# Performance work log

Hardware: AMD Instinct MI355X
Metric: run time of the kernel (lower is better)

## Reference

```python
import jax, jax.numpy as jnp
import numpy as np

B, S, E, H, FFN, NQ, DEPTH = 2, 2048, 1024, 16, 4096, 4, 2
DK = E // H
LN_EPS = 1e-5


def _layernorm(t, g, b):
    m = t.mean(-1, keepdims=True)
    v = ((t - m) ** 2).mean(-1, keepdims=True)
    return (t - m) / jnp.sqrt(v + LN_EPS) * g + b


def setup_inputs() -> dict:
    key = jax.random.key(0)
    ks = jax.random.split(key, 12)
    n = lambda i, shape, sc=1.0: (jax.random.normal(ks[i], shape, jnp.float32) * sc)
    return {
        "x": n(0, (B, S, E)),
        "wq": n(1, (E, E), 0.02),
        "wk": n(2, (E, E), 0.02),
        "wv": n(3, (E, E), 0.02),
        "wo": n(4, (E, E), 0.02),
        "w1": n(5, (E, FFN), 0.02),
        "b1": jnp.zeros((FFN,), jnp.float32),
        "w2": n(6, (FFN, E), 0.02),
        "b2": jnp.zeros((E,), jnp.float32),
        "qp_attn": n(7, (NQ, DEPTH)),
        "qp_ffn": n(8, (NQ, DEPTH)),
        "ln1_g": jnp.ones((E,), jnp.float32),
        "ln1_b": jnp.zeros((E,), jnp.float32),
        "ln2_g": jnp.ones((E,), jnp.float32),
        "ln2_b": jnp.zeros((E,), jnp.float32),
    }


def reference(x, wq, wk, wv, wo, w1, b1, w2, b2, qp_attn, qp_ffn,
              ln1_g, ln1_b, ln2_g, ln2_b):
    b, s, _ = x.shape
    # --- quantum attention ---
    q = (x @ wq).reshape(b, s, H, DK)
    k = (x @ wk).reshape(b, s, H, DK)
    v = (x @ wv).reshape(b, s, H, DK)
    scores = jnp.einsum('bqhd,bkhd->bhqk', q, k) / np.sqrt(DK).astype(np.float32)
    attn = jax.nn.softmax(scores, axis=-1)
    classical = jnp.einsum('bhqk,bkhd->bqhd', attn, v)  # (b, s, H, DK)
    # depth-2 RX-only circuit on |0..0>: <Z_0> = cos(sum_d params[0, d]);
    # data-independent scalar broadcast to the first NQ channels of each head
    c_attn = jnp.cos(qp_attn[0].sum())
    mixed = classical.at[..., :NQ].add(c_attn)
    attn_out = mixed.reshape(b, s, E) @ wo
    x1 = _layernorm(x + attn_out, ln1_g, ln1_b)  # dropout is identity in eval
    # --- quantum feed-forward ---
    h = x1 @ w1 + b1  # computed in the source but never consumed by the circuit
    # depth-2 RY-only circuit: <Z_0> = cos(sum_d params[0, d]) -- also data-free
    c_ffn = jnp.cos(qp_ffn[0].sum())
    qvec = jnp.zeros((FFN,), x.dtype).at[:NQ].set(c_ffn)
    ffn_out = jax.nn.relu(qvec) @ w2 + b2  # (E,), broadcast per token
    return _layernorm(x1 + ffn_out, ln2_g, ln2_b)
```

## Files before the change

kernel.cpp:

```cpp
#include <hip/hip_runtime.h>
#include <hip/hip_bf16.h>

typedef unsigned short u16;
using short8 = __attribute__((ext_vector_type(8))) short;
using f32x4  = __attribute__((ext_vector_type(4))) float;

#define S_  2048
#define E_  1024
#define H_  16
#define DK_ 64

#define GLP(p)  ((const __attribute__((address_space(1))) void*)(p))
#define LDSP(p) ((__attribute__((address_space(3))) void*)(p))

__device__ __forceinline__ float b2f(u16 u) {
  union { unsigned int i; float f; } v; v.i = ((unsigned int)u) << 16; return v.f;
}
__device__ __forceinline__ u16 f2b(float f) {
  union { float f; unsigned int i; } v; v.f = f;
  unsigned int r = v.i + 0x7fffu + ((v.i >> 16) & 1u);
  return (u16)(r >> 16);
}
__device__ __forceinline__ unsigned pk2(float a, float b) {
  __hip_bfloat162 h = __float22bfloat162_rn(make_float2(a, b));
  union { __hip_bfloat162 h; unsigned u; } c; c.h = h; return c.u;
}

__global__ __launch_bounds__(256) void prep_k(
    const float* __restrict__ x,
    const float* __restrict__ wq, const float* __restrict__ wk,
    const float* __restrict__ wv, const float* __restrict__ wo,
    const float* __restrict__ w2, const float* __restrict__ b2,
    const float* __restrict__ qpf,
    u16* __restrict__ xb, u16* __restrict__ wt, float* __restrict__ fv) {
  __shared__ u16 tile[64][65];
  int id = blockIdx.x, t = threadIdx.x;
  if (id < 2048) {
    size_t i = ((size_t)id * 256 + t) * 8;
    float4 a = *(const float4*)&x[i];
    float4 b = *(const float4*)&x[i + 4];
    uint4 o;
    o.x = pk2(a.x, a.y); o.y = pk2(a.z, a.w);
    o.z = pk2(b.x, b.y); o.w = pk2(b.z, b.w);
    *(uint4*)&xb[i] = o;
  } else if (id < 3072) {
    int i = id - 2048;
    int z = i >> 8; i &= 255;
    const float* src = (z == 0) ? wq : (z == 1) ? wk : (z == 2) ? wv : wo;
    u16* dst = wt + (size_t)z * E_ * E_;
    int k0 = (i & 15) * 64, n0 = (i >> 4) * 64;
    int rr = t >> 4, c4 = (t & 15) * 4;
    for (int p = 0; p < 4; p++) {
      int r = p * 16 + rr;
      float4 v = *(const float4*)&src[(size_t)(k0 + r) * E_ + n0 + c4];
      tile[r][c4] = f2b(v.x); tile[r][c4 + 1] = f2b(v.y);
      tile[r][c4 + 2] = f2b(v.z); tile[r][c4 + 3] = f2b(v.w);
    }
    __syncthreads();
    for (int p = 0; p < 4; p++) {
      int r = p * 16 + rr;
      ushort4 o;
      o.x = tile[c4][r]; o.y = tile[c4 + 1][r]; o.z = tile[c4 + 2][r]; o.w = tile[c4 + 3][r];
      *(ushort4*)&dst[(size_t)(n0 + r) * E_ + k0 + c4] = o;
    }
  } else {
    int e = (id - 3072) * 256 + t;
    float r = fmaxf(cosf(qpf[0] + qpf[1]), 0.f);
    fv[e] = b2[e] + r * (w2[0 * E_ + e] + w2[1 * E_ + e] + w2[2 * E_ + e] + w2[3 * E_ + e]);
  }
}

__device__ __forceinline__ void gemm_loop97(
    const u16* __restrict__ A, const u16* __restrict__ Bt,
    int m0, int n0, f32x4 acc[4][4], u16 (*As)[128][32], u16 (*Bs)[128][32]) {
  int t = threadIdx.x, lane = t & 63, w = t >> 6;
  int wm = w >> 1, wn = w & 1, l15 = lane & 15, quad = lane >> 4;
  int srow = lane >> 2, sch = (lane & 3) * 8;
  const u16 *ga[2], *gb[2];
#pragma unroll
  for (int p = 0; p < 2; p++) {
    int seg = w * 2 + p;
    ga[p] = A + (size_t)(m0 + seg * 16 + srow) * E_ + sch;
    gb[p] = Bt + (size_t)(n0 + seg * 16 + srow) * E_ + sch;
  }
#pragma unroll
  for (int p = 0; p < 2; p++) {
    int seg = w * 2 + p;
    __builtin_amdgcn_global_load_lds(GLP(ga[p]), LDSP(&As[0][seg * 16][0]), 16, 0, 0);
    __builtin_amdgcn_global_load_lds(GLP(gb[p]), LDSP(&Bs[0][seg * 16][0]), 16, 0, 0);
    ga[p] += 32; gb[p] += 32;
  }
  for (int i = 0; i < 32; i++) {
    __syncthreads();
    if (i + 1 < 32) {
      int nb = (i + 1) & 1;
#pragma unroll
      for (int p = 0; p < 2; p++) {
        int seg = w * 2 + p;
        __builtin_amdgcn_global_load_lds(GLP(ga[p]), LDSP(&As[nb][seg * 16][0]), 16, 0, 0);
        __builtin_amdgcn_global_load_lds(GLP(gb[p]), LDSP(&Bs[nb][seg * 16][0]), 16, 0, 0);
        ga[p] += 32; gb[p] += 32;
      }
    }
    int cb = i & 1;
    short8 af[4], bf[4];
#pragma unroll
    for (int ii = 0; ii < 4; ii++) af[ii] = *(const short8*)&As[cb][wm * 64 + ii * 16 + l15][quad * 8];
#pragma unroll
    for (int j = 0; j < 4; j++) bf[j] = *(const short8*)&Bs[cb][wn * 64 + j * 16 + l15][quad * 8];
#pragma unroll
    for (int ii = 0; ii < 4; ii++)
#pragma unroll
      for (int j = 0; j < 4; j++)
        acc[ii][j] = __builtin_amdgcn_mfma_f32_16x16x32_bf16(af[ii], bf[j], acc[ii][j], 0, 0, 0);
  }
}

__global__ __launch_bounds__(256) void qkv_gemm(
    const u16* __restrict__ xb, const u16* __restrict__ wt,
    u16* __restrict__ q, u16* __restrict__ k, u16* __restrict__ vt) {
  __shared__ __align__(16) u16 As[2][128][32];
  __shared__ __align__(16) u16 Bs[2][128][32];
  int n0 = blockIdx.x * 128, m0 = blockIdx.y * 128, z = blockIdx.z;
  const u16* Bt = wt + (size_t)z * E_ * E_;
  f32x4 acc[4][4];
  f32x4 zero = {0.f, 0.f, 0.f, 0.f};
  for (int i = 0; i < 4; i++)
    for (int j = 0; j < 4; j++) acc[i][j] = zero;
  gemm_loop97(xb, Bt, m0, n0, acc, As, Bs);
  int t = threadIdx.x, lane = t & 63, w = t >> 6;
  int wm = w >> 1, wn = w & 1, l15 = lane & 15, quad = lane >> 4;
  if (z < 2) {
    u16* out = (z == 0) ? q : k;
    float sc = (z == 0) ? 0.125f : 1.f;
#pragma unroll
    for (int i = 0; i < 4; i++)
#pragma unroll
      for (int j = 0; j < 4; j++) {
        int mm = m0 + wm * 64 + i * 16 + quad * 4;
        int nn = n0 + wn * 64 + j * 16 + l15;
#pragma unroll
        for (int rr = 0; rr < 4; rr++)
          out[(size_t)(mm + rr) * E_ + nn] = f2b(acc[i][j][rr] * sc);
      }
  } else {
#pragma unroll
    for (int i = 0; i < 4; i++)
#pragma unroll
      for (int j = 0; j < 4; j++) {
        int mm = m0 + wm * 64 + i * 16 + quad * 4;
        int nn = n0 + wn * 64 + j * 16 + l15;
        int b = mm >> 11, s = mm & (S_ - 1);
        size_t base = ((size_t)(b * H_ + (nn >> 6)) * DK_ + (nn & 63)) * S_ + s;
        ushort4 pk;
        pk.x = f2b(acc[i][j][0]); pk.y = f2b(acc[i][j][1]);
        pk.z = f2b(acc[i][j][2]); pk.w = f2b(acc[i][j][3]);
        *(ushort4*)&vt[base] = pk;
      }
  }
}

__global__ __launch_bounds__(256) void oproj_gemm(
    const u16* __restrict__ am, const u16* __restrict__ wot, float* __restrict__ proj) {
  __shared__ __align__(16) u16 As[2][128][32];
  __shared__ __align__(16) u16 Bs[2][128][32];
  int n0 = blockIdx.x * 128, m0 = blockIdx.y * 128;
  f32x4 acc[4][4];
  f32x4 zero = {0.f, 0.f, 0.f, 0.f};
  for (int i = 0; i < 4; i++)
    for (int j = 0; j < 4; j++) acc[i][j] = zero;
  gemm_loop97(am, wot, m0, n0, acc, As, Bs);
  int t = threadIdx.x, lane = t & 63, w = t >> 6;
  int wm = w >> 1, wn = w & 1, l15 = lane & 15, quad = lane >> 4;
#pragma unroll
  for (int i = 0; i < 4; i++)
#pragma unroll
    for (int j = 0; j < 4; j++) {
      int mm = m0 + wm * 64 + i * 16 + quad * 4;
      int nn = n0 + wn * 64 + j * 16 + l15;
#pragma unroll
      for (int rr = 0; rr < 4; rr++)
        proj[(size_t)(mm + rr) * E_ + nn] = acc[i][j][rr];
    }
}

__global__ __launch_bounds__(256) void attn_kernel(
    const u16* __restrict__ q, const u16* __restrict__ kk,
    const u16* __restrict__ vt, const float* __restrict__ qpa,
    u16* __restrict__ outm) {
  __shared__ __align__(16) u16 Qs[64][64];
  __shared__ __align__(16) u16 Ks[2][64][64];
  __shared__ __align__(16) u16 Vts[2][64][64];
  __shared__ __align__(16) u16 Ps[4][16][72];
  int qt = blockIdx.x, bh = blockIdx.y;
  int b = bh >> 4, h = bh & 15;
  int q0 = qt * 64;
  int t = threadIdx.x, lane = t & 63, w = t >> 6;
  int l15 = lane & 15, quad = lane >> 4;
  float c_attn = cosf(qpa[0] + qpa[1]);
  int sr = lane >> 3, slot = lane & 7;
  size_t kbase = (size_t)(b * S_) * E_ + h * DK_;
  size_t vbase = (size_t)(b * H_ + h) * DK_ * S_;
  const u16 *kptr[2], *vptr[2];
#pragma unroll
  for (int p = 0; p < 2; p++) {
    int seg = w * 2 + p;
    int r = seg * 8 + sr;
    int c = slot ^ (r & 7);
    const u16* gq = q + (size_t)(b * S_ + q0 + r) * E_ + h * DK_ + c * 8;
    __builtin_amdgcn_global_load_lds(GLP(gq), LDSP(&Qs[seg * 8][0]), 16, 0, 0);
    kptr[p] = kk + kbase + (size_t)r * E_ + c * 8;
    vptr[p] = vt + vbase + (size_t)r * S_ + c * 8;
    __builtin_amdgcn_global_load_lds(GLP(kptr[p]), LDSP(&Ks[0][seg * 8][0]), 16, 0, 0);
    __builtin_amdgcn_global_load_lds(GLP(vptr[p]), LDSP(&Vts[0][seg * 8][0]), 16, 0, 0);
    kptr[p] += (size_t)64 * E_;
    vptr[p] += 64;
  }
  __syncthreads();
  int rowq = w * 16 + l15;
  int cq = quad ^ (rowq & 7);
  short8 aq0 = *(const short8*)&Qs[rowq][cq * 8];
  short8 aq1 = *(const short8*)&Qs[rowq][(cq ^ 4) * 8];
  f32x4 O[4];
  float lrunL[4];
  f32x4 zero = {0.f, 0.f, 0.f, 0.f};
  for (int i = 0; i < 4; i++) { O[i] = zero; lrunL[i] = 0.f; }
  for (int kt = 0; kt < S_ / 64; kt++) {
    if (kt) __syncthreads();
    if (kt + 1 < S_ / 64) {
      int nb = (kt + 1) & 1;
#pragma unroll
      for (int p = 0; p < 2; p++) {
        int seg = w * 2 + p;
        __builtin_amdgcn_global_load_lds(GLP(kptr[p]), LDSP(&Ks[nb][seg * 8][0]), 16, 0, 0);
        __builtin_amdgcn_global_load_lds(GLP(vptr[p]), LDSP(&Vts[nb][seg * 8][0]), 16, 0, 0);
        kptr[p] += (size_t)64 * E_;
        vptr[p] += 64;
      }
    }
    int cb = kt & 1;
    f32x4 sc[4];
#pragma unroll
    for (int nt = 0; nt < 4; nt++) {
      int row = nt * 16 + l15;
      int ck = quad ^ (row & 7);
      short8 bk0 = *(const short8*)&Ks[cb][row][ck * 8];
      short8 bk1 = *(const short8*)&Ks[cb][row][(ck ^ 4) * 8];
      f32x4 z = zero;
      z = __builtin_amdgcn_mfma_f32_16x16x32_bf16(aq0, bk0, z, 0, 0, 0);
      z = __builtin_amdgcn_mfma_f32_16x16x32_bf16(aq1, bk1, z, 0, 0, 0);
      sc[nt] = z;
    }
#pragma unroll
    for (int r = 0; r < 4; r++) {
      float p0 = __expf(fminf(sc[0][r], 30.f));
      float p1 = __expf(fminf(sc[1][r], 30.f));
      float p2 = __expf(fminf(sc[2][r], 30.f));
      float p3 = __expf(fminf(sc[3][r], 30.f));
      unsigned pa = pk2(p0, p1), pb = pk2(p2, p3);
      u16* prow = &Ps[w][quad * 4 + r][l15];
      prow[0]  = (u16)pa; prow[16] = (u16)(pa >> 16);
      prow[32] = (u16)pb; prow[48] = (u16)(pb >> 16);
      lrunL[r] += (p0 + p1) + (p2 + p3);
    }
    asm volatile("s_waitcnt lgkmcnt(0)" ::: "memory");
    short8 ap0 = *(const short8*)&Ps[w][l15][quad * 8];
    short8 ap1 = *(const short8*)&Ps[w][l15][32 + quad * 8];
#pragma unroll
    for (int nt = 0; nt < 4; nt++) {
      int row = nt * 16 + l15;
      int cv = quad ^ (row & 7);
      short8 bv0 = *(const short8*)&Vts[cb][row][cv * 8];
      short8 bv1 = *(const short8*)&Vts[cb][row][(cv ^ 4) * 8];
      O[nt] = __builtin_amdgcn_mfma_f32_16x16x32_bf16(ap0, bv0, O[nt], 0, 0, 0);
      O[nt] = __builtin_amdgcn_mfma_f32_16x16x32_bf16(ap1, bv1, O[nt], 0, 0, 0);
    }
  }
  float inv[4];
#pragma unroll
  for (int r = 0; r < 4; r++) {
    float rs = lrunL[r];
#pragma unroll
    for (int msk = 1; msk < 16; msk <<= 1) rs += __shfl_xor(rs, msk, 64);
    inv[r] = 1.f / rs;
  }
#pragma unroll
  for (int nt = 0; nt < 4; nt++)
#pragma unroll
    for (int r = 0; r < 4; r++) {
      float val = O[nt][r] * inv[r];
      int d = nt * 16 + l15;
      if (d < 4) val += c_attn;
      int tok = b * S_ + q0 + w * 16 + quad * 4 + r;
      outm[(size_t)tok * E_ + h * DK_ + d] = f2b(val);
    }
}

__global__ __launch_bounds__(256) void ln_fused(
    const float* __restrict__ x, const float* __restrict__ proj, const float* __restrict__ fv,
    const float* __restrict__ g1, const float* __restrict__ bb1,
    const float* __restrict__ g2, const float* __restrict__ bb2,
    float* __restrict__ out) {
  __shared__ float sm[8];
  int tok = blockIdx.x, t = threadIdx.x;
  int e0 = t * 4;
  float4 xv = *(const float4*)&x[(size_t)tok * E_ + e0];
  float4 pv = *(const float4*)&proj[(size_t)tok * E_ + e0];
  float v0 = xv.x + pv.x, v1 = xv.y + pv.y;
  float v2 = xv.z + pv.z, v3 = xv.w + pv.w;
  float s = v0 + v1 + v2 + v3;
  float sq = v0 * v0 + v1 * v1 + v2 * v2 + v3 * v3;
  for (int m = 32; m >= 1; m >>= 1) { s += __shfl_xor(s, m, 64); sq += __shfl_xor(sq, m, 64); }
  int wid = t >> 6, lane = t & 63;
  if (lane == 0) { sm[wid] = s; sm[4 + wid] = sq; }
  __syncthreads();
  s = sm[0] + sm[1] + sm[2] + sm[3];
  sq = sm[4] + sm[5] + sm[6] + sm[7];
  float mean = s * (1.f / E_);
  float var = sq * (1.f / E_) - mean * mean;
  float rstd = rsqrtf(var + 1e-5f);
  float4 g1v = *(const float4*)&g1[e0];
  float4 b1v = *(const float4*)&bb1[e0];
  float4 fvv = *(const float4*)&fv[e0];
  float t0 = (v0 - mean) * rstd * g1v.x + b1v.x + fvv.x;
  float t1 = (v1 - mean) * rstd * g1v.y + b1v.y + fvv.y;
  float t2 = (v2 - mean) * rstd * g1v.z + b1v.z + fvv.z;
  float t3 = (v3 - mean) * rstd * g1v.w + b1v.w + fvv.w;
  float s2 = t0 + t1 + t2 + t3;
  float sq2 = t0 * t0 + t1 * t1 + t2 * t2 + t3 * t3;
  for (int m = 32; m >= 1; m >>= 1) { s2 += __shfl_xor(s2, m, 64); sq2 += __shfl_xor(sq2, m, 64); }
  __syncthreads();
  if (lane == 0) { sm[wid] = s2; sm[4 + wid] = sq2; }
  __syncthreads();
  s2 = sm[0] + sm[1] + sm[2] + sm[3];
  sq2 = sm[4] + sm[5] + sm[6] + sm[7];
  float mean2 = s2 * (1.f / E_);
  float var2 = sq2 * (1.f / E_) - mean2 * mean2;
  float rstd2 = rsqrtf(var2 + 1e-5f);
  float4 g2v = *(const float4*)&g2[e0];
  float4 b2v = *(const float4*)&bb2[e0];
  float4 ov;
  ov.x = (t0 - mean2) * rstd2 * g2v.x + b2v.x;
  ov.y = (t1 - mean2) * rstd2 * g2v.y + b2v.y;
  ov.z = (t2 - mean2) * rstd2 * g2v.z + b2v.z;
  ov.w = (t3 - mean2) * rstd2 * g2v.w + b2v.w;
  *(float4*)&out[(size_t)tok * E_ + e0] = ov;
}

extern "C" void kernel_launch(void* const* d_in, const int* in_sizes, int n_in,
                              void* d_out, int out_size, void* d_ws, size_t ws_size,
                              hipStream_t stream) {
  const float* x   = (const float*)d_in[0];
  const float* wq  = (const float*)d_in[1];
  const float* wk  = (const float*)d_in[2];
  const float* wv  = (const float*)d_in[3];
  const float* wo  = (const float*)d_in[4];
  const float* w2  = (const float*)d_in[7];
  const float* b2  = (const float*)d_in[8];
  const float* qpa = (const float*)d_in[9];
  const float* qpf = (const float*)d_in[10];
  const float* g1  = (const float*)d_in[11];
  const float* bb1 = (const float*)d_in[12];
  const float* g2  = (const float*)d_in[13];
  const float* bb2 = (const float*)d_in[14];

  char* ws = (char*)d_ws;
  u16* wt     = (u16*)ws;
  u16* q      = (u16*)(ws + (size_t)8  * 1048576);
  u16* k      = (u16*)(ws + (size_t)16 * 1048576);
  float* proj = (float*)(ws + (size_t)8 * 1048576);
  float* fv   = (float*)(ws + (size_t)24 * 1048576);
  u16* xb     = (u16*)d_out;
  u16* am     = (u16*)d_out;
  u16* vt     = (u16*)d_out + (size_t)4 * 1048576;
  float* outp = (float*)d_out;

  prep_k<<<dim3(3076), 256, 0, stream>>>(x, wq, wk, wv, wo, w2, b2, qpf, xb, wt, fv);
  qkv_gemm<<<dim3(8, 32, 3), 256, 0, stream>>>(xb, wt, q, k, vt);
  attn_kernel<<<dim3(32, 32), 256, 0, stream>>>(q, k, vt, qpa, am);
  oproj_gemm<<<dim3(8, 32), 256, 0, stream>>>(am, wt + (size_t)3 * E_ * E_, proj);
  ln_fused<<<dim3(4096), 256, 0, stream>>>(x, proj, fv, g1, bb1, g2, bb2, outp);
}
```

Measured before the change: 279.5 us.

## Double attention query tile to 128 rows per block and swap MFMA operand roles

Each attention block now handles 128 query rows instead of 64, with every wave owning 32 query rows. Each K/V tile loaded into LDS is therefore reused across twice as many queries, halving global K/V traffic and the number of blocks. The score MFMA is transposed (K as A operand, Q as B) so P is written to LDS as packed 8-byte stores with an XOR swizzle, and row sums are reduced through LDS. Costs are more registers per wave (launch_bounds 256,2), only 512 blocks in the grid, and more complex indexing.

After: 260.8 us. 1.07x faster.

```diff
diff --git a/kernel.cpp b/kernel.cpp
--- a/kernel.cpp
+++ b/kernel.cpp
@@ -184,116 +184,149 @@
     }
 }
 
-__global__ __launch_bounds__(256) void attn_kernel(
+__global__ __launch_bounds__(256, 2) void attn_kernel(
     const u16* __restrict__ q, const u16* __restrict__ kk,
     const u16* __restrict__ vt, const float* __restrict__ qpa,
     u16* __restrict__ outm) {
-  __shared__ __align__(16) u16 Qs[64][64];
+  __shared__ __align__(16) u16 Qs[128][64];
   __shared__ __align__(16) u16 Ks[2][64][64];
   __shared__ __align__(16) u16 Vts[2][64][64];
-  __shared__ __align__(16) u16 Ps[4][16][72];
+  __shared__ __align__(16) u16 Ps[4][32][64];
+  __shared__ float Ls[4][32];
   int qt = blockIdx.x, bh = blockIdx.y;
   int b = bh >> 4, h = bh & 15;
-  int q0 = qt * 64;
+  int q0 = qt * 128;
   int t = threadIdx.x, lane = t & 63, w = t >> 6;
   int l15 = lane & 15, quad = lane >> 4;
   float c_attn = cosf(qpa[0] + qpa[1]);
-  int sr = lane >> 3, slot = lane & 7;
+  int r8 = lane >> 3, slot = lane & 7;
   size_t kbase = (size_t)(b * S_) * E_ + h * DK_;
   size_t vbase = (size_t)(b * H_ + h) * DK_ * S_;
+#pragma unroll
+  for (int p = 0; p < 4; p++) {
+    int row = w * 32 + p * 8 + r8;
+    int c = slot ^ (row & 7);
+    const u16* gq = q + (size_t)(b * S_ + q0 + row) * E_ + h * DK_ + c * 8;
+    __builtin_amdgcn_global_load_lds(GLP(gq), LDSP(&Qs[w * 32 + p * 8][0]), 16, 0, 0);
+  }
   const u16 *kptr[2], *vptr[2];
 #pragma unroll
   for (int p = 0; p < 2; p++) {
-    int seg = w * 2 + p;
-    int r = seg * 8 + sr;
-    int c = slot ^ (r & 7);
-    const u16* gq = q + (size_t)(b * S_ + q0 + r) * E_ + h * DK_ + c * 8;
-    __builtin_amdgcn_global_load_lds(GLP(gq), LDSP(&Qs[seg * 8][0]), 16, 0, 0);
-    kptr[p] = kk + kbase + (size_t)r * E_ + c * 8;
-    vptr[p] = vt + vbase + (size_t)r * S_ + c * 8;
-    __builtin_amdgcn_global_load_lds(GLP(kptr[p]), LDSP(&Ks[0][seg * 8][0]), 16, 0, 0);
-    __builtin_amdgcn_global_load_lds(GLP(vptr[p]), LDSP(&Vts[0][seg * 8][0]), 16, 0, 0);
+    int row = w * 16 + p * 8 + r8;
+    int c = slot ^ (row & 7);
+    kptr[p] = kk + kbase + (size_t)row * E_ + c * 8;
+    vptr[p] = vt + vbase + (size_t)row * S_ + c * 8;
+    __builtin_amdgcn_global_load_lds(GLP(kptr[p]), LDSP(&Ks[0][w * 16 + p * 8][0]), 16, 0, 0);
+    __builtin_amdgcn_global_load_lds(GLP(vptr[p]), LDSP(&Vts[0][w * 16 + p * 8][0]), 16, 0, 0);
     kptr[p] += (size_t)64 * E_;
     vptr[p] += 64;
   }
   __syncthreads();
-  int rowq = w * 16 + l15;
-  int cq = quad ^ (rowq & 7);
-  short8 aq0 = *(const short8*)&Qs[rowq][cq * 8];
-  short8 aq1 = *(const short8*)&Qs[rowq][(cq ^ 4) * 8];
-  f32x4 O[4];
-  float lrunL[4];
+  short8 bq[2][2];
+#pragma unroll
+  for (int nb = 0; nb < 2; nb++) {
+    int row = w * 32 + nb * 16 + l15;
+    int c0 = quad ^ (row & 7);
+    bq[nb][0] = *(const short8*)&Qs[row][c0 * 8];
+    bq[nb][1] = *(const short8*)&Qs[row][(c0 ^ 4) * 8];
+  }
+  f32x4 O[2][4];
+  float lrun[2] = {0.f, 0.f};
   f32x4 zero = {0.f, 0.f, 0.f, 0.f};
-  for (int i = 0; i < 4; i++) { O[i] = zero; lrunL[i] = 0.f; }
+#pragma unroll
+  for (int i = 0; i < 2; i++)
+#pragma unroll
+    for (int j = 0; j < 4; j++) O[i][j] = zero;
   for (int kt = 0; kt < S_ / 64; kt++) {
     if (kt) __syncthreads();
     if (kt + 1 < S_ / 64) {
-      int nb = (kt + 1) & 1;
+      int nb2 = (kt + 1) & 1;
 #pragma unroll
       for (int p = 0; p < 2; p++) {
-        int seg = w * 2 + p;
-        __builtin_amdgcn_global_load_lds(GLP(kptr[p]), LDSP(&Ks[nb][seg * 8][0]), 16, 0, 0);
-        __builtin_amdgcn_global_load_lds(GLP(vptr[p]), LDSP(&Vts[nb][seg * 8][0]), 16, 0, 0);
+        __builtin_amdgcn_global_load_lds(GLP(kptr[p]), LDSP(&Ks[nb2][w * 16 + p * 8][0]), 16, 0, 0);
+        __builtin_amdgcn_global_load_lds(GLP(vptr[p]), LDSP(&Vts[nb2][w * 16 + p * 8][0]), 16, 0, 0);
         kptr[p] += (size_t)64 * E_;
         vptr[p] += 64;
       }
     }
     int cb = kt & 1;
-    f32x4 sc[4];
-#pragma unroll
-    for (int nt = 0; nt < 4; nt++) {
-      int row = nt * 16 + l15;
-      int ck = quad ^ (row & 7);
-      short8 bk0 = *(const short8*)&Ks[cb][row][ck * 8];
-      short8 bk1 = *(const short8*)&Ks[cb][row][(ck ^ 4) * 8];
-      f32x4 z = zero;
-      z = __builtin_amdgcn_mfma_f32_16x16x32_bf16(aq0, bk0, z, 0, 0, 0);
-      z = __builtin_amdgcn_mfma_f32_16x16x32_bf16(aq1, bk1, z, 0, 0, 0);
-      sc[nt] = z;
-    }
-#pragma unroll
-    for (int r = 0; r < 4; r++) {
-      float p0 = __expf(fminf(sc[0][r], 30.f));
-      float p1 = __expf(fminf(sc[1][r], 30.f));
-      float p2 = __expf(fminf(sc[2][r], 30.f));
-      float p3 = __expf(fminf(sc[3][r], 30.f));
-      unsigned pa = pk2(p0, p1), pb = pk2(p2, p3);
-      u16* prow = &Ps[w][quad * 4 + r][l15];
-      prow[0]  = (u16)pa; prow[16] = (u16)(pa >> 16);
-      prow[32] = (u16)pb; prow[48] = (u16)(pb >> 16);
-      lrunL[r] += (p0 + p1) + (p2 + p3);
-    }
+    f32x4 sc[4][2];
+#pragma unroll
+    for (int mb = 0; mb < 4; mb++) {
+      int row = mb * 16 + l15;
+      int c0 = quad ^ (row & 7);
+      short8 a0 = *(const short8*)&Ks[cb][row][c0 * 8];
+      short8 a1 = *(const short8*)&Ks[cb][row][(c0 ^ 4) * 8];
+#pragma unroll
+      for (int nb = 0; nb < 2; nb++) {
+        f32x4 z = __builtin_amdgcn_mfma_f32_16x16x32_bf16(a0, bq[nb][0], zero, 0, 0, 0);
+        sc[mb][nb] = __builtin_amdgcn_mfma_f32_16x16x32_bf16(a1, bq[nb][1], z, 0, 0, 0);
+      }
+    }
+#pragma unroll
+    for (int mb = 0; mb < 4; mb++)
+#pragma unroll
+      for (int nb = 0; nb < 2; nb++) {
+        float p0 = __expf(fminf(sc[mb][nb][0], 30.f));
+        float p1 = __expf(fminf(sc[mb][nb][1], 30.f));
+        float p2 = __expf(fminf(sc[mb][nb][2], 30.f));
+        float p3 = __expf(fminf(sc[mb][nb][3], 30.f));
+        lrun[nb] += (p0 + p1) + (p2 + p3);
+        unsigned pa = pk2(p0, p1), pb = pk2(p2, p3);
+        int row = nb * 16 + l15;
+        int cch = (mb * 2 + (quad >> 1)) ^ (row & 7);
+        uint2 pw; pw.x = pa; pw.y = pb;
+        *(uint2*)&Ps[w][row][cch * 8 + (quad & 1) * 4] = pw;
+      }
     asm volatile("s_waitcnt lgkmcnt(0)" ::: "memory");
-    short8 ap0 = *(const short8*)&Ps[w][l15][quad * 8];
-    short8 ap1 = *(const short8*)&Ps[w][l15][32 + quad * 8];
-#pragma unroll
-    for (int nt = 0; nt < 4; nt++) {
-      int row = nt * 16 + l15;
-      int cv = quad ^ (row & 7);
-      short8 bv0 = *(const short8*)&Vts[cb][row][cv * 8];
-      short8 bv1 = *(const short8*)&Vts[cb][row][(cv ^ 4) * 8];
-      O[nt] = __builtin_amdgcn_mfma_f32_16x16x32_bf16(ap0, bv0, O[nt], 0, 0, 0);
-      O[nt] = __builtin_amdgcn_mfma_f32_16x16x32_bf16(ap1, bv1, O[nt], 0, 0, 0);
-    }
-  }
-  float inv[4];
-#pragma unroll
-  for (int r = 0; r < 4; r++) {
-    float rs = lrunL[r];
-#pragma unroll
-    for (int msk = 1; msk < 16; msk <<= 1) rs += __shfl_xor(rs, msk, 64);
-    inv[r] = 1.f / rs;
-  }
-#pragma unroll
-  for (int nt = 0; nt < 4; nt++)
-#pragma unroll
-    for (int r = 0; r < 4; r++) {
-      float val = O[nt][r] * inv[r];
-      int d = nt * 16 + l15;
-      if (d < 4) val += c_attn;
-      int tok = b * S_ + q0 + w * 16 + quad * 4 + r;
-      outm[(size_t)tok * E_ + h * DK_ + d] = f2b(val);
-    }
+    short8 bv[4][2];
+#pragma unroll
+    for (int nd = 0; nd < 4; nd++) {
+      int rv = nd * 16 + l15;
+      int cv = quad ^ (rv & 7);
+      bv[nd][0] = *(const short8*)&Vts[cb][rv][cv * 8];
+      bv[nd][1] = *(const short8*)&Vts[cb][rv][(cv ^ 4) * 8];
+    }
+#pragma unroll
+    for (int mbq = 0; mbq < 2; mbq++) {
+      int row = mbq * 16 + l15;
+      int s0 = quad ^ (row & 7);
+      int s1 = (4 + quad) ^ (row & 7);
+      short8 ap0 = *(const short8*)&Ps[w][row][s0 * 8];
+      short8 ap1 = *(const short8*)&Ps[w][row][s1 * 8];
+#pragma unroll
+      for (int nd = 0; nd < 4; nd++) {
+        O[mbq][nd] = __builtin_amdgcn_mfma_f32_16x16x32_bf16(ap0, bv[nd][0], O[mbq][nd], 0, 0, 0);
+        O[mbq][nd] = __builtin_amdgcn_mfma_f32_16x16x32_bf16(ap1, bv[nd][1], O[mbq][nd], 0, 0, 0);
+      }
+    }
+  }
+#pragma unroll
+  for (int nb = 0; nb < 2; nb++) {
+    float rs = lrun[nb];
+    rs += __shfl_xor(rs, 16, 64);
+    rs += __shfl_xor(rs, 32, 64);
+    Ls[w][nb * 16 + l15] = rs;
+  }
+  asm volatile("s_waitcnt lgkmcnt(0)" ::: "memory");
+  float inv[2][4];
+#pragma unroll
+  for (int mbq = 0; mbq < 2; mbq++)
+#pragma unroll
+    for (int r = 0; r < 4; r++)
+      inv[mbq][r] = 1.f / Ls[w][mbq * 16 + quad * 4 + r];
+#pragma unroll
+  for (int mbq = 0; mbq < 2; mbq++)
+#pragma unroll
+    for (int nd = 0; nd < 4; nd++)
+#pragma unroll
+      for (int r = 0; r < 4; r++) {
+        float val = O[mbq][nd][r] * inv[mbq][r];
+        int d = nd * 16 + l15;
+        if (nd == 0 && l15 < 4) val += c_attn;
+        int tok = b * S_ + q0 + w * 32 + mbq * 16 + quad * 4 + r;
+        outm[(size_t)tok * E_ + h * DK_ + d] = f2b(val);
+      }
 }
 
 __global__ __launch_bounds__(256) void ln_fused(
@@ -377,7 +410,7 @@
 
   prep_k<<<dim3(3076), 256, 0, stream>>>(x, wq, wk, wv, wo, w2, b2, qpf, xb, wt, fv);
   qkv_gemm<<<dim3(8, 32, 3), 256, 0, stream>>>(xb, wt, q, k, vt);
-  attn_kernel<<<dim3(32, 32), 256, 0, stream>>>(q, k, vt, qpa, am);
+  attn_kernel<<<dim3(16, 32), 256, 0, stream>>>(q, k, vt, qpa, am);
   oproj_gemm<<<dim3(8, 32), 256, 0, stream>>>(am, wt + (size_t)3 * E_ * E_, proj);
   ln_fused<<<dim3(4096), 256, 0, stream>>>(x, proj, fv, g1, bb1, g2, bb2, outp);
 }
```
